# Optimization experiments

Hardware: AMD Instinct MI355X
Metric: run time of the kernel (lower is better)

Reference implementation:

```python
import jax, jax.numpy as jnp
import numpy as np

N = 50000        # n_nodes
E = 800000       # n_edges (avg degree 16)
H = 64           # hidden_size
ALPHA = 0.5      # CRF alpha
BETA = 0.5       # CRF beta
N_LAYER = 2      # args.crf_layer
GAMMA = 0.2      # LeakyReLU negative slope


def setup_inputs() -> dict:
    key = jax.random.key(0)
    k = jax.random.split(key, 5)
    emb = jax.random.normal(k[0], (N, H), jnp.float32)
    W_fc = jax.random.normal(k[1], (H, H), jnp.float32) / np.sqrt(H)
    attn_fc_w = jax.random.normal(k[2], (1, 2 * H), jnp.float32) / np.sqrt(2 * H)
    src = jax.random.randint(k[3], (E,), 0, N, dtype=jnp.int32)
    dst = jax.random.randint(k[4], (E,), 0, N, dtype=jnp.int32)
    return {"emb": emb, "W_fc": W_fc, "attn_fc_w": attn_fc_w, "src": src, "dst": dst}


def _segment_softmax(e, dst, n):
    # softmax over incoming edges of each destination node (DGL mailbox softmax)
    m = jax.ops.segment_max(e, dst, num_segments=n)
    m = jnp.where(jnp.isfinite(m), m, 0.0)  # nodes with no in-edges
    ex = jnp.exp(e - m[dst])
    denom = jax.ops.segment_sum(ex, dst, num_segments=n)
    return ex / jnp.maximum(denom[dst], 1e-16)


def reference(emb, W_fc, attn_fc_w, src, dst):
    # attn_fc(concat(z_src, z_dst)) split into two per-node projections
    a_src = attn_fc_w[0, :H]
    a_dst = attn_fc_w[0, H:]
    h = emb
    e = None
    for _ in range(N_LAYER):
        z = h @ W_fc.T                              # [N, H] emb_attn
        e = (z @ a_src)[src] + (z @ a_dst)[dst]     # [E] edge logits
        e = jnp.where(e > 0, e, GAMMA * e)          # LeakyReLU(gamma)
        att = _segment_softmax(e, dst, N)           # [E]
        crf = jax.ops.segment_sum(att[:, None] * h[src], dst, num_segments=N)  # [N, H]
        h = (ALPHA * emb + BETA * crf) / (ALPHA + BETA)
    # training loss (is_train=True); reuses last layer's edge logits e
    loss_a = jnp.sum((h - emb) ** 2, axis=-1)                     # [N]
    att = _segment_softmax(e, dst, N)
    diff = jnp.sqrt(jnp.sum((h[dst] - h[src]) ** 2, axis=-1) + 1e-12)  # [E] L2 norm
    loss_b = jax.ops.segment_sum(att * diff, dst, num_segments=N)  # [N]
    loss = jnp.mean(ALPHA * loss_a + BETA * loss_b)
    return h, loss
```

## Files before the change

kernel.cpp:

```cpp
#include <hip/hip_runtime.h>

#define NNODES 50000
#define NEDGES 800000
#define HDIM 64
#define CAP 64
#define GAMMA 0.2f
#define INIT_B 256
#define INIT_NB ((NNODES + INIT_B - 1) / INIT_B)
#define NPART 8
#define NODES_PER_PART ((NNODES + NPART - 1) / NPART)
#define FILL_SLICES 192
#define E4 (NEDGES / 4)
#define CHUNK ((E4 + FILL_SLICES - 1) / FILL_SLICES)
#define NB ((NNODES + 3) / 4)

typedef unsigned short u16;
typedef unsigned int u32;

__device__ __forceinline__ u16 f2bf(float f) {
    u32 u = __float_as_uint(f);
    u32 r = (u + 0x7FFFu + ((u >> 16) & 1u)) >> 16;
    return (u16)r;
}
__device__ __forceinline__ float bflo(u32 u) { return __uint_as_float(u << 16); }
__device__ __forceinline__ float bfhi(u32 u) { return __uint_as_float(u & 0xFFFF0000u); }

__device__ __forceinline__ float wave_sum(float v) {
    #pragma unroll
    for (int off = 32; off; off >>= 1) v += __shfl_xor(v, off, 64);
    return v;
}
__device__ __forceinline__ float wave_max(float v) {
    #pragma unroll
    for (int off = 32; off; off >>= 1) v = fmaxf(v, __shfl_xor(v, off, 64));
    return v;
}
__device__ __forceinline__ float group8_sum(float v) {
    v += __shfl_xor(v, 1, 64);
    v += __shfl_xor(v, 2, 64);
    v += __shfl_xor(v, 4, 64);
    return v;
}

__global__ __launch_bounds__(256) void k_init(int* __restrict__ cursor,
                                              const float* __restrict__ Wfc,
                                              const float* __restrict__ attn,
                                              float* __restrict__ ws, float* __restrict__ wd) {
    int t = threadIdx.x;
    int idx = blockIdx.x * 256 + t;
    if (idx < NNODES) cursor[idx] = 0;
    if (blockIdx.x == gridDim.x - 1) {
        if (t >= 128) {
            int tt = t - 128;
            int k = tt & 63;
            const float* av = attn + ((tt >= 64) ? HDIM : 0);
            float s = 0.f;
            for (int j = 0; j < HDIM; ++j) s += Wfc[j * HDIM + k] * av[j];
            if (tt < 64) ws[k] = s; else wd[k] = s;
        }
    }
}

__global__ __launch_bounds__(256) void k_fillx(const int4* __restrict__ src4,
                                               const int4* __restrict__ dst4,
                                               int* __restrict__ cursor,
                                               u16* __restrict__ padded) {
    const int part = blockIdx.x & (NPART - 1);
    const int slice = blockIdx.x >> 3;
    const int lo = slice * CHUNK;
    const int hi = min(lo + CHUNK, E4);
    const int plo = part * NODES_PER_PART;
    const int phi = plo + NODES_PER_PART;
    for (int i = lo + threadIdx.x; i < hi; i += 256) {
        int4 d = dst4[i];
        bool mx = d.x >= plo && d.x < phi;
        bool my = d.y >= plo && d.y < phi;
        bool mz = d.z >= plo && d.z < phi;
        bool mw = d.w >= plo && d.w < phi;
        if (mx | my | mz | mw) {
            int4 s = src4[i];
            if (mx) { int p0 = atomicAdd(&cursor[d.x], 1); if (p0 < CAP) padded[d.x * CAP + p0] = (u16)s.x; }
            if (my) { int p1 = atomicAdd(&cursor[d.y], 1); if (p1 < CAP) padded[d.y * CAP + p1] = (u16)s.y; }
            if (mz) { int p2 = atomicAdd(&cursor[d.z], 1); if (p2 < CAP) padded[d.z * CAP + p2] = (u16)s.z; }
            if (mw) { int p3 = atomicAdd(&cursor[d.w], 1); if (p3 < CAP) padded[d.w * CAP + p3] = (u16)s.w; }
        }
    }
}

__global__ __launch_bounds__(256) void k_zinit(const float* __restrict__ emb,
                                               const float* __restrict__ ws,
                                               const float* __restrict__ wd,
                                               u16* __restrict__ emb_bf,
                                               float* __restrict__ zs, float* __restrict__ zd) {
    int tid = blockIdx.x * blockDim.x + threadIdx.x;
    int wid = tid >> 6;
    int lane = tid & 63;
    if (wid < NNODES) {
        float v = emb[wid * HDIM + lane];
        emb_bf[wid * HDIM + lane] = f2bf(v);
        float a = wave_sum(v * ws[lane]);
        float b = wave_sum(v * wd[lane]);
        if (lane == 0) { zs[wid] = a; zd[wid] = b; }
    }
}

template <bool COMPUTE_Z, bool WRITE_F32, bool STORE_LA>
__global__ __launch_bounds__(256) void k_layer(const u16* __restrict__ hbf_in,
                                               const float* __restrict__ emb,
                                               const int* __restrict__ deg,
                                               const u16* __restrict__ padded,
                                               const float* __restrict__ zs,
                                               const float* __restrict__ zd,
                                               float* __restrict__ h_out,
                                               u16* __restrict__ hbf_out,
                                               const float* __restrict__ ws,
                                               const float* __restrict__ wd,
                                               float* __restrict__ zs_out,
                                               float* __restrict__ zd_out,
                                               float* __restrict__ la) {
    int wid = (blockIdx.x * blockDim.x + threadIdx.x) >> 6;
    int lane = threadIdx.x & 63;
    if (wid >= NNODES) return;
    int ne = min(deg[wid], CAP);
    float zdn = zd[wid];
    const int sub8 = lane >> 3, q8 = lane & 7;
    float acc[8];
    #pragma unroll
    for (int i = 0; i < 8; ++i) acc[i] = 0.f;

    int s = 0; float e = -INFINITY;
    bool valid = lane < ne;
    if (valid) {
        s = padded[(size_t)wid * CAP + lane];
        float z = zs[s] + zdn;
        e = z > 0.f ? z : GAMMA * z;
    }
    float m = wave_max(e);
    float ex = valid ? __expf(e - m) : 0.f;
    float dsum = wave_sum(ex);
    float inv = 1.f / fmaxf(dsum, 1e-16f);
    for (int j = 0; j < ne; j += 16) {
        int ja = j + sub8, jb = j + 8 + sub8;
        float wa = __shfl(ex, ja, 64);
        float wb = __shfl(ex, jb, 64);
        int ta = __shfl(s, ja, 64);
        int tb = __shfl(s, jb, 64);
        const uint4 ra = *(const uint4*)&hbf_in[(size_t)ta * HDIM + 8 * q8];
        const uint4 rb = *(const uint4*)&hbf_in[(size_t)tb * HDIM + 8 * q8];
        acc[0] += wa * bflo(ra.x) + wb * bflo(rb.x);
        acc[1] += wa * bfhi(ra.x) + wb * bfhi(rb.x);
        acc[2] += wa * bflo(ra.y) + wb * bflo(rb.y);
        acc[3] += wa * bfhi(ra.y) + wb * bfhi(rb.y);
        acc[4] += wa * bflo(ra.z) + wb * bflo(rb.z);
        acc[5] += wa * bfhi(ra.z) + wb * bfhi(rb.z);
        acc[6] += wa * bflo(ra.w) + wb * bflo(rb.w);
        acc[7] += wa * bfhi(ra.w) + wb * bfhi(rb.w);
    }
    #pragma unroll
    for (int off = 8; off <= 32; off <<= 1) {
        #pragma unroll
        for (int i = 0; i < 8; ++i) acc[i] += __shfl_xor(acc[i], off, 64);
    }
    float hv[8];
    #pragma unroll
    for (int i = 0; i < 8; ++i) hv[i] = 0.f;
    float lap = 0.f;
    if (sub8 == 0) {
        const float4 e0 = *(const float4*)&emb[(size_t)wid * HDIM + 8 * q8];
        const float4 e1 = *(const float4*)&emb[(size_t)wid * HDIM + 8 * q8 + 4];
        hv[0] = 0.5f * (e0.x + acc[0] * inv);
        hv[1] = 0.5f * (e0.y + acc[1] * inv);
        hv[2] = 0.5f * (e0.z + acc[2] * inv);
        hv[3] = 0.5f * (e0.w + acc[3] * inv);
        hv[4] = 0.5f * (e1.x + acc[4] * inv);
        hv[5] = 0.5f * (e1.y + acc[5] * inv);
        hv[6] = 0.5f * (e1.z + acc[6] * inv);
        hv[7] = 0.5f * (e1.w + acc[7] * inv);
        if (WRITE_F32) {
            *(float4*)&h_out[(size_t)wid * HDIM + 8 * q8]     = make_float4(hv[0], hv[1], hv[2], hv[3]);
            *(float4*)&h_out[(size_t)wid * HDIM + 8 * q8 + 4] = make_float4(hv[4], hv[5], hv[6], hv[7]);
        }
        uint4 o;
        o.x = (u32)f2bf(hv[0]) | ((u32)f2bf(hv[1]) << 16);
        o.y = (u32)f2bf(hv[2]) | ((u32)f2bf(hv[3]) << 16);
        o.z = (u32)f2bf(hv[4]) | ((u32)f2bf(hv[5]) << 16);
        o.w = (u32)f2bf(hv[6]) | ((u32)f2bf(hv[7]) << 16);
        *(uint4*)&hbf_out[(size_t)wid * HDIM + 8 * q8] = o;
        if (STORE_LA) {
            float d0 = hv[0] - e0.x, d1 = hv[1] - e0.y, d2 = hv[2] - e0.z, d3 = hv[3] - e0.w;
            float d4 = hv[4] - e1.x, d5 = hv[5] - e1.y, d6 = hv[6] - e1.z, d7 = hv[7] - e1.w;
            lap = d0 * d0 + d1 * d1 + d2 * d2 + d3 * d3 +
                  d4 * d4 + d5 * d5 + d6 * d6 + d7 * d7;
        }
    }
    if (STORE_LA) {
        float lsum = wave_sum(lap);
        if (lane == 0) la[wid] = lsum;
    }
    if (COMPUTE_Z) {
        float pa = 0.f, pb = 0.f;
        if (sub8 == 0) {
            const float4 w0 = *(const float4*)&ws[8 * q8];
            const float4 w1 = *(const float4*)&ws[8 * q8 + 4];
            const float4 d0 = *(const float4*)&wd[8 * q8];
            const float4 d1 = *(const float4*)&wd[8 * q8 + 4];
            pa = hv[0] * w0.x + hv[1] * w0.y + hv[2] * w0.z + hv[3] * w0.w +
                 hv[4] * w1.x + hv[5] * w1.y + hv[6] * w1.z + hv[7] * w1.w;
            pb = hv[0] * d0.x + hv[1] * d0.y + hv[2] * d0.z + hv[3] * d0.w +
                 hv[4] * d1.x + hv[5] * d1.y + hv[6] * d1.z + hv[7] * d1.w;
        }
        float a = wave_sum(pa);
        float b = wave_sum(pb);
        if (lane == 0) { zs_out[wid] = a; zd_out[wid] = b; }
    }
}

__global__ __launch_bounds__(256) void k_loss(const float* __restrict__ la,
                                              const u16* __restrict__ hbf,
                                              const int* __restrict__ deg,
                                              const u16* __restrict__ padded,
                                              const float* __restrict__ zs,
                                              const float* __restrict__ zd,
                                              float* __restrict__ partials) {
    const int lane = threadIdx.x & 63;
    const int wib = threadIdx.x >> 6;
    const int gtid = blockIdx.x * blockDim.x + threadIdx.x;
    const int nthreads = gridDim.x * blockDim.x;
    const int wid = gtid >> 6;
    const int sub8 = lane >> 3, q8 = lane & 7;
    float lb = 0.f;

    for (int i = gtid; i < NNODES / 4; i += nthreads) {
        const float4 v = *(const float4*)&la[i * 4];
        lb += 0.5f * (v.x + v.y + v.z + v.w);
    }

    if (wid < NNODES) {
        int ne = min(deg[wid], CAP);
        if (ne > 0) {
            float zdn = zd[wid];
            int s = 0; float e = -INFINITY;
            bool valid = lane < ne;
            if (valid) {
                s = padded[(size_t)wid * CAP + lane];
                float z = zs[s] + zdn;
                e = z > 0.f ? z : GAMMA * z;
            }
            float m = wave_max(e);
            float ex = valid ? __expf(e - m) : 0.f;
            float dsum = wave_sum(ex);
            float att = ex * (1.f / fmaxf(dsum, 1e-16f));
            const uint4 rd = *(const uint4*)&hbf[(size_t)wid * HDIM + 8 * q8];
            const float h0 = bflo(rd.x), h1 = bfhi(rd.x), h2 = bflo(rd.y), h3 = bfhi(rd.y);
            const float h4 = bflo(rd.z), h5 = bfhi(rd.z), h6 = bflo(rd.w), h7 = bfhi(rd.w);
            float part = 0.f;
            for (int j = 0; j < ne; j += 16) {
                int ja = j + sub8, jb = j + 8 + sub8;
                float wa = __shfl(att, ja, 64);
                float wb = __shfl(att, jb, 64);
                int ta = __shfl(s, ja, 64);
                int tb = __shfl(s, jb, 64);
                const uint4 ra = *(const uint4*)&hbf[(size_t)ta * HDIM + 8 * q8];
                const uint4 rb = *(const uint4*)&hbf[(size_t)tb * HDIM + 8 * q8];
                float a0 = bflo(ra.x) - h0, a1 = bfhi(ra.x) - h1;
                float a2 = bflo(ra.y) - h2, a3 = bfhi(ra.y) - h3;
                float a4 = bflo(ra.z) - h4, a5 = bfhi(ra.z) - h5;
                float a6 = bflo(ra.w) - h6, a7 = bfhi(ra.w) - h7;
                float b0 = bflo(rb.x) - h0, b1 = bfhi(rb.x) - h1;
                float b2 = bflo(rb.y) - h2, b3 = bfhi(rb.y) - h3;
                float b4 = bflo(rb.z) - h4, b5 = bfhi(rb.z) - h5;
                float b6 = bflo(rb.w) - h6, b7 = bfhi(rb.w) - h7;
                float ssa = group8_sum(a0 * a0 + a1 * a1 + a2 * a2 + a3 * a3 +
                                       a4 * a4 + a5 * a5 + a6 * a6 + a7 * a7);
                float ssb = group8_sum(b0 * b0 + b1 * b1 + b2 * b2 + b3 * b3 +
                                       b4 * b4 + b5 * b5 + b6 * b6 + b7 * b7);
                if (q8 == 0) part += wa * sqrtf(ssa + 1e-12f) + wb * sqrtf(ssb + 1e-12f);
            }
            lb += 0.5f * part;
        }
    }
    lb = wave_sum(lb);
    __shared__ float psum[4];
    if (lane == 0) psum[wib] = lb;
    __syncthreads();
    if (threadIdx.x == 0)
        partials[blockIdx.x] = psum[0] + psum[1] + psum[2] + psum[3];
}

__global__ __launch_bounds__(256) void k_finalize(const float* __restrict__ partials,
                                                  float* __restrict__ out_loss) {
    const int t = threadIdx.x;
    const int lane = t & 63;
    const int wib = t >> 6;
    float v = 0.f;
    for (int i = t; i < NB; i += 256) v += partials[i];
    v = wave_sum(v);
    __shared__ float psum[4];
    if (lane == 0) psum[wib] = v;
    __syncthreads();
    if (t == 0) out_loss[0] = (psum[0] + psum[1] + psum[2] + psum[3]) / (float)NNODES;
}

extern "C" void kernel_launch(void* const* d_in, const int* in_sizes, int n_in,
                              void* d_out, int out_size, void* d_ws, size_t ws_size,
                              hipStream_t stream) {
    const float* emb  = (const float*)d_in[0];
    const float* Wfc  = (const float*)d_in[1];
    const float* attn = (const float*)d_in[2];
    const int*   src  = (const int*)d_in[3];
    const int*   dst  = (const int*)d_in[4];
    float* out = (float*)d_out;

    char* p = (char*)d_ws;
    int*   cursor  = (int*)p;   p += (size_t)NNODES * 4;
    float* wsv     = (float*)p; p += 64 * 4;
    float* wdv     = (float*)p; p += 64 * 4;
    float* zs0     = (float*)p; p += (size_t)NNODES * 4;
    float* zd0     = (float*)p; p += (size_t)NNODES * 4;
    float* zs1     = (float*)p; p += (size_t)NNODES * 4;
    float* zd1     = (float*)p; p += (size_t)NNODES * 4;
    float* laArr   = (float*)p; p += (size_t)NNODES * 4;
    float* partials= (float*)p; p += (size_t)NB * 4;
    p = (char*)(((size_t)p + 255) & ~(size_t)255);
    u16*   padded  = (u16*)p;   p += (size_t)NNODES * CAP * 2;
    u16*   emb_bf  = (u16*)p;   p += (size_t)NNODES * HDIM * 2;
    u16*   h1_bf   = (u16*)p;   p += (size_t)NNODES * HDIM * 2;
    u16*   out_bf  = (u16*)p;   p += (size_t)NNODES * HDIM * 2;

    k_init<<<INIT_NB, 256, 0, stream>>>(cursor, Wfc, attn, wsv, wdv);
    k_fillx<<<NPART * FILL_SLICES, 256, 0, stream>>>((const int4*)src, (const int4*)dst,
                                                     cursor, padded);
    k_zinit<<<NB, 256, 0, stream>>>(emb, wsv, wdv, emb_bf, zs0, zd0);

    k_layer<true, false, false><<<NB, 256, 0, stream>>>(
        emb_bf, emb, cursor, padded, zs0, zd0,
        out , h1_bf, wsv, wdv, zs1, zd1, laArr);
    k_layer<false, true, true><<<NB, 256, 0, stream>>>(
        h1_bf, emb, cursor, padded, zs1, zd1,
        out, out_bf, wsv, wdv, zs0, zd0, laArr);

    k_loss<<<NB, 256, 0, stream>>>(laArr, out_bf, cursor, padded, zs1, zd1, partials);
    k_finalize<<<1, 256, 0, stream>>>(partials, out + (size_t)NNODES * HDIM);
}
```

Measured before the change: 226.7 us.

## Fuse z-init into edge fill kernel and reduce loss_a per block

The per-node bf16 conversion and attention-projection pass moves from its own kernel into the tail of the edge-bucketing kernel, using a grid-stride loop over nodes. This removes one kernel launch. The second layer now reduces the squared-difference loss term per block into a partials array, so the per-node loss array is no longer written and then reread by the loss kernel. The finalize kernel combines both partial arrays. Correctness relies on the node count filling the blocks exactly, because a `__syncthreads` now follows an early-return path and the bounds check was dropped from the loss kernel.

Result: no change. 225.2 us (-0.7%).

```diff
diff --git a/kernel.cpp b/kernel.cpp
--- a/kernel.cpp
+++ b/kernel.cpp
@@ -64,7 +64,13 @@
 __global__ __launch_bounds__(256) void k_fillx(const int4* __restrict__ src4,
                                                const int4* __restrict__ dst4,
                                                int* __restrict__ cursor,
-                                               u16* __restrict__ padded) {
+                                               u16* __restrict__ padded,
+                                               const float* __restrict__ emb,
+                                               const float* __restrict__ ws,
+                                               const float* __restrict__ wd,
+                                               u16* __restrict__ emb_bf,
+                                               float* __restrict__ zs,
+                                               float* __restrict__ zd) {
     const int part = blockIdx.x & (NPART - 1);
     const int slice = blockIdx.x >> 3;
     const int lo = slice * CHUNK;
@@ -85,22 +91,16 @@
             if (mw) { int p3 = atomicAdd(&cursor[d.w], 1); if (p3 < CAP) padded[d.w * CAP + p3] = (u16)s.w; }
         }
     }
-}
-
-__global__ __launch_bounds__(256) void k_zinit(const float* __restrict__ emb,
-                                               const float* __restrict__ ws,
-                                               const float* __restrict__ wd,
-                                               u16* __restrict__ emb_bf,
-                                               float* __restrict__ zs, float* __restrict__ zd) {
-    int tid = blockIdx.x * blockDim.x + threadIdx.x;
-    int wid = tid >> 6;
-    int lane = tid & 63;
-    if (wid < NNODES) {
-        float v = emb[wid * HDIM + lane];
-        emb_bf[wid * HDIM + lane] = f2bf(v);
-        float a = wave_sum(v * ws[lane]);
-        float b = wave_sum(v * wd[lane]);
-        if (lane == 0) { zs[wid] = a; zd[wid] = b; }
+    const int lane = threadIdx.x & 63;
+    const int gw = (blockIdx.x * 256 + threadIdx.x) >> 6;
+    const int nw = (gridDim.x * 256) >> 6;
+    const float wsl = ws[lane], wdl = wd[lane];
+    for (int n = gw; n < NNODES; n += nw) {
+        float v = emb[n * HDIM + lane];
+        emb_bf[n * HDIM + lane] = f2bf(v);
+        float a = wave_sum(v * wsl);
+        float b = wave_sum(v * wdl);
+        if (lane == 0) { zs[n] = a; zd[n] = b; }
     }
 }
 
@@ -117,7 +117,7 @@
                                                const float* __restrict__ wd,
                                                float* __restrict__ zs_out,
                                                float* __restrict__ zd_out,
-                                               float* __restrict__ la) {
+                                               float* __restrict__ partialsA) {
     int wid = (blockIdx.x * blockDim.x + threadIdx.x) >> 6;
     int lane = threadIdx.x & 63;
     if (wid >= NNODES) return;
@@ -195,7 +195,11 @@
     }
     if (STORE_LA) {
         float lsum = wave_sum(lap);
-        if (lane == 0) la[wid] = lsum;
+        __shared__ float ps[4];
+        if (lane == 0) ps[threadIdx.x >> 6] = lsum;
+        __syncthreads();
+        if (threadIdx.x == 0)
+            partialsA[blockIdx.x] = ps[0] + ps[1] + ps[2] + ps[3];
     }
     if (COMPUTE_Z) {
         float pa = 0.f, pb = 0.f;
@@ -215,86 +219,77 @@
     }
 }
 
-__global__ __launch_bounds__(256) void k_loss(const float* __restrict__ la,
-                                              const u16* __restrict__ hbf,
+__global__ __launch_bounds__(256) void k_loss(const u16* __restrict__ hbf,
                                               const int* __restrict__ deg,
                                               const u16* __restrict__ padded,
                                               const float* __restrict__ zs,
                                               const float* __restrict__ zd,
-                                              float* __restrict__ partials) {
+                                              float* __restrict__ partialsB) {
     const int lane = threadIdx.x & 63;
     const int wib = threadIdx.x >> 6;
-    const int gtid = blockIdx.x * blockDim.x + threadIdx.x;
-    const int nthreads = gridDim.x * blockDim.x;
-    const int wid = gtid >> 6;
+    const int wid = (blockIdx.x * blockDim.x + threadIdx.x) >> 6;
     const int sub8 = lane >> 3, q8 = lane & 7;
     float lb = 0.f;
 
-    for (int i = gtid; i < NNODES / 4; i += nthreads) {
-        const float4 v = *(const float4*)&la[i * 4];
-        lb += 0.5f * (v.x + v.y + v.z + v.w);
-    }
-
-    if (wid < NNODES) {
-        int ne = min(deg[wid], CAP);
-        if (ne > 0) {
-            float zdn = zd[wid];
-            int s = 0; float e = -INFINITY;
-            bool valid = lane < ne;
-            if (valid) {
-                s = padded[(size_t)wid * CAP + lane];
-                float z = zs[s] + zdn;
-                e = z > 0.f ? z : GAMMA * z;
-            }
-            float m = wave_max(e);
-            float ex = valid ? __expf(e - m) : 0.f;
-            float dsum = wave_sum(ex);
-            float att = ex * (1.f / fmaxf(dsum, 1e-16f));
-            const uint4 rd = *(const uint4*)&hbf[(size_t)wid * HDIM + 8 * q8];
-            const float h0 = bflo(rd.x), h1 = bfhi(rd.x), h2 = bflo(rd.y), h3 = bfhi(rd.y);
-            const float h4 = bflo(rd.z), h5 = bfhi(rd.z), h6 = bflo(rd.w), h7 = bfhi(rd.w);
-            float part = 0.f;
-            for (int j = 0; j < ne; j += 16) {
-                int ja = j + sub8, jb = j + 8 + sub8;
-                float wa = __shfl(att, ja, 64);
-                float wb = __shfl(att, jb, 64);
-                int ta = __shfl(s, ja, 64);
-                int tb = __shfl(s, jb, 64);
-                const uint4 ra = *(const uint4*)&hbf[(size_t)ta * HDIM + 8 * q8];
-                const uint4 rb = *(const uint4*)&hbf[(size_t)tb * HDIM + 8 * q8];
-                float a0 = bflo(ra.x) - h0, a1 = bfhi(ra.x) - h1;
-                float a2 = bflo(ra.y) - h2, a3 = bfhi(ra.y) - h3;
-                float a4 = bflo(ra.z) - h4, a5 = bfhi(ra.z) - h5;
-                float a6 = bflo(ra.w) - h6, a7 = bfhi(ra.w) - h7;
-                float b0 = bflo(rb.x) - h0, b1 = bfhi(rb.x) - h1;
-                float b2 = bflo(rb.y) - h2, b3 = bfhi(rb.y) - h3;
-                float b4 = bflo(rb.z) - h4, b5 = bfhi(rb.z) - h5;
-                float b6 = bflo(rb.w) - h6, b7 = bfhi(rb.w) - h7;
-                float ssa = group8_sum(a0 * a0 + a1 * a1 + a2 * a2 + a3 * a3 +
-                                       a4 * a4 + a5 * a5 + a6 * a6 + a7 * a7);
-                float ssb = group8_sum(b0 * b0 + b1 * b1 + b2 * b2 + b3 * b3 +
-                                       b4 * b4 + b5 * b5 + b6 * b6 + b7 * b7);
-                if (q8 == 0) part += wa * sqrtf(ssa + 1e-12f) + wb * sqrtf(ssb + 1e-12f);
-            }
-            lb += 0.5f * part;
-        }
+    int ne = min(deg[wid], CAP);
+    if (ne > 0) {
+        const uint4 rd = *(const uint4*)&hbf[(size_t)wid * HDIM + 8 * q8];
+        float zdn = zd[wid];
+        int s = 0; float e = -INFINITY;
+        bool valid = lane < ne;
+        if (valid) {
+            s = padded[(size_t)wid * CAP + lane];
+            float z = zs[s] + zdn;
+            e = z > 0.f ? z : GAMMA * z;
+        }
+        float m = wave_max(e);
+        float ex = valid ? __expf(e - m) : 0.f;
+        float dsum = wave_sum(ex);
+        float att = ex * (1.f / fmaxf(dsum, 1e-16f));
+        const float h0 = bflo(rd.x), h1 = bfhi(rd.x), h2 = bflo(rd.y), h3 = bfhi(rd.y);
+        const float h4 = bflo(rd.z), h5 = bfhi(rd.z), h6 = bflo(rd.w), h7 = bfhi(rd.w);
+        float part = 0.f;
+        for (int j = 0; j < ne; j += 16) {
+            int ja = j + sub8, jb = j + 8 + sub8;
+            float wa = __shfl(att, ja, 64);
+            float wb = __shfl(att, jb, 64);
+            int ta = __shfl(s, ja, 64);
+            int tb = __shfl(s, jb, 64);
+            const uint4 ra = *(const uint4*)&hbf[(size_t)ta * HDIM + 8 * q8];
+            const uint4 rb = *(const uint4*)&hbf[(size_t)tb * HDIM + 8 * q8];
+            float a0 = bflo(ra.x) - h0, a1 = bfhi(ra.x) - h1;
+            float a2 = bflo(ra.y) - h2, a3 = bfhi(ra.y) - h3;
+            float a4 = bflo(ra.z) - h4, a5 = bfhi(ra.z) - h5;
+            float a6 = bflo(ra.w) - h6, a7 = bfhi(ra.w) - h7;
+            float b0 = bflo(rb.x) - h0, b1 = bfhi(rb.x) - h1;
+            float b2 = bflo(rb.y) - h2, b3 = bfhi(rb.y) - h3;
+            float b4 = bflo(rb.z) - h4, b5 = bfhi(rb.z) - h5;
+            float b6 = bflo(rb.w) - h6, b7 = bfhi(rb.w) - h7;
+            float ssa = group8_sum(a0 * a0 + a1 * a1 + a2 * a2 + a3 * a3 +
+                                   a4 * a4 + a5 * a5 + a6 * a6 + a7 * a7);
+            float ssb = group8_sum(b0 * b0 + b1 * b1 + b2 * b2 + b3 * b3 +
+                                   b4 * b4 + b5 * b5 + b6 * b6 + b7 * b7);
+            if (q8 == 0) part += wa * sqrtf(ssa + 1e-12f) + wb * sqrtf(ssb + 1e-12f);
+        }
+        lb = 0.5f * part;
     }
     lb = wave_sum(lb);
     __shared__ float psum[4];
     if (lane == 0) psum[wib] = lb;
     __syncthreads();
     if (threadIdx.x == 0)
-        partials[blockIdx.x] = psum[0] + psum[1] + psum[2] + psum[3];
-}
-
-__global__ __launch_bounds__(256) void k_finalize(const float* __restrict__ partials,
+        partialsB[blockIdx.x] = psum[0] + psum[1] + psum[2] + psum[3];
+}
+
+__global__ __launch_bounds__(256) void k_finalize(const float* __restrict__ partialsA,
+                                                  const float* __restrict__ partialsB,
                                                   float* __restrict__ out_loss) {
     const int t = threadIdx.x;
     const int lane = t & 63;
     const int wib = t >> 6;
-    float v = 0.f;
-    for (int i = t; i < NB; i += 256) v += partials[i];
-    v = wave_sum(v);
+    float va = 0.f, vb = 0.f;
+    for (int i = t; i < NB; i += 256) { va += partialsA[i]; vb += partialsB[i]; }
+    float v = wave_sum(0.5f * va + vb);
     __shared__ float psum[4];
     if (lane == 0) psum[wib] = v;
     __syncthreads();
@@ -312,33 +307,33 @@
     float* out = (float*)d_out;
 
     char* p = (char*)d_ws;
-    int*   cursor  = (int*)p;   p += (size_t)NNODES * 4;
-    float* wsv     = (float*)p; p += 64 * 4;
-    float* wdv     = (float*)p; p += 64 * 4;
-    float* zs0     = (float*)p; p += (size_t)NNODES * 4;
-    float* zd0     = (float*)p; p += (size_t)NNODES * 4;
-    float* zs1     = (float*)p; p += (size_t)NNODES * 4;
-    float* zd1     = (float*)p; p += (size_t)NNODES * 4;
-    float* laArr   = (float*)p; p += (size_t)NNODES * 4;
-    float* partials= (float*)p; p += (size_t)NB * 4;
+    int*   cursor   = (int*)p;   p += (size_t)NNODES * 4;
+    float* wsv      = (float*)p; p += 64 * 4;
+    float* wdv      = (float*)p; p += 64 * 4;
+    float* zs0      = (float*)p; p += (size_t)NNODES * 4;
+    float* zd0      = (float*)p; p += (size_t)NNODES * 4;
+    float* zs1      = (float*)p; p += (size_t)NNODES * 4;
+    float* zd1      = (float*)p; p += (size_t)NNODES * 4;
+    float* partialsA= (float*)p; p += (size_t)NB * 4;
+    float* partialsB= (float*)p; p += (size_t)NB * 4;
     p = (char*)(((size_t)p + 255) & ~(size_t)255);
-    u16*   padded  = (u16*)p;   p += (size_t)NNODES * CAP * 2;
-    u16*   emb_bf  = (u16*)p;   p += (size_t)NNODES * HDIM * 2;
-    u16*   h1_bf   = (u16*)p;   p += (size_t)NNODES * HDIM * 2;
-    u16*   out_bf  = (u16*)p;   p += (size_t)NNODES * HDIM * 2;
+    u16*   padded   = (u16*)p;   p += (size_t)NNODES * CAP * 2;
+    u16*   emb_bf   = (u16*)p;   p += (size_t)NNODES * HDIM * 2;
+    u16*   h1_bf    = (u16*)p;   p += (size_t)NNODES * HDIM * 2;
+    u16*   out_bf   = (u16*)p;   p += (size_t)NNODES * HDIM * 2;
 
     k_init<<<INIT_NB, 256, 0, stream>>>(cursor, Wfc, attn, wsv, wdv);
     k_fillx<<<NPART * FILL_SLICES, 256, 0, stream>>>((const int4*)src, (const int4*)dst,
-                                                     cursor, padded);
-    k_zinit<<<NB, 256, 0, stream>>>(emb, wsv, wdv, emb_bf, zs0, zd0);
+                                                     cursor, padded,
+                                                     emb, wsv, wdv, emb_bf, zs0, zd0);
 
     k_layer<true, false, false><<<NB, 256, 0, stream>>>(
         emb_bf, emb, cursor, padded, zs0, zd0,
-        out , h1_bf, wsv, wdv, zs1, zd1, laArr);
+        out , h1_bf, wsv, wdv, zs1, zd1, partialsA);
     k_layer<false, true, true><<<NB, 256, 0, stream>>>(
         h1_bf, emb, cursor, padded, zs1, zd1,
-        out, out_bf, wsv, wdv, zs0, zd0, laArr);
-
-    k_loss<<<NB, 256, 0, stream>>>(laArr, out_bf, cursor, padded, zs1, zd1, partials);
-    k_finalize<<<1, 256, 0, stream>>>(partials, out + (size_t)NNODES * HDIM);
-}
+        out, out_bf, wsv, wdv, zs0, zd0, partialsA);
+
+    k_loss<<<NB, 256, 0, stream>>>(out_bf, cursor, padded, zs1, zd1, partialsB);
+    k_finalize<<<1, 256, 0, stream>>>(partialsA, partialsB, out + (size_t)NNODES * HDIM);
+}
```
